# Kernel optimization log

Hardware: AMD Instinct MI355X
Metric: run time of the kernel (lower is better)

The kernel has to match this reference:

```python
import jax, jax.numpy as jnp
import numpy as np

N, E, F_IN, NCLS, H = 50000, 800000, 128, 10, 64


def setup_inputs() -> dict:
    key = jax.random.key(0)
    ks = jax.random.split(key, 24)
    p = lambda k, shp: (jax.random.normal(k, shp, dtype=jnp.float32) * 0.1)
    inp = {
        'x': jax.random.normal(ks[0], (N, F_IN), dtype=jnp.float32),
        'edge_index': jax.random.randint(ks[1], (2, E), 0, N, dtype=jnp.int64),
        'gcn1_W': p(ks[2], (F_IN, 128)), 'gcn1_b': p(ks[3], (128,)),
        'gcn2_W': p(ks[4], (128, 64)),  'gcn2_b': p(ks[5], (64,)),
        'gcn3_W': p(ks[6], (64, 32)),   'gcn3_b': p(ks[7], (32,)),
        'gat_W': p(ks[8], (32, 32)), 'gat_a_src': p(ks[9], (32,)),
        'gat_a_dst': p(ks[10], (32,)), 'gat_b': p(ks[11], (32,)),
        'lstm_Wih_f': p(ks[12], (4 * H, 32)), 'lstm_bih_f': p(ks[13], (4 * H,)), 'lstm_bhh_f': p(ks[14], (4 * H,)),
        'lstm_Wih_b': p(ks[15], (4 * H, 32)), 'lstm_bih_b': p(ks[16], (4 * H,)), 'lstm_bhh_b': p(ks[17], (4 * H,)),
        'bn_gamma': jnp.ones((2 * H,), jnp.float32), 'bn_beta': jnp.zeros((2 * H,), jnp.float32),
        'fc_W': p(ks[18], (NCLS, 2 * H)), 'fc_b': p(ks[19], (NCLS,)),
    }
    return inp


def _forward(x, edge_index, gcn1_W, gcn1_b, gcn2_W, gcn2_b, gcn3_W, gcn3_b,
             gat_W, gat_a_src, gat_a_dst, gat_b,
             lstm_Wih_f, lstm_bih_f, lstm_bhh_f, lstm_Wih_b, lstm_bih_b, lstm_bhh_b,
             bn_gamma, bn_beta, fc_W, fc_b):
    n = x.shape[0]
    loop = jnp.arange(n)
    row = jnp.concatenate([edge_index[0], loop])  # source nodes (+ self loops)
    col = jnp.concatenate([edge_index[1], loop])  # target nodes
    deg = jax.ops.segment_sum(jnp.ones_like(col, dtype=x.dtype), col, num_segments=n)
    dis = jax.lax.rsqrt(jnp.maximum(deg, 1e-12))  # deg >= 1 due to self loops
    norm = dis[row] * dis[col]

    def gcn(h, W, b):
        h = h @ W
        return jax.ops.segment_sum(h[row] * norm[:, None], col, num_segments=n) + b

    h = jax.nn.relu(gcn(x, gcn1_W, gcn1_b))
    h = jax.nn.relu(gcn(h, gcn2_W, gcn2_b))
    h = gcn(h, gcn3_W, gcn3_b)

    # GAT (1 head), self loops already in row/col, softmax over incoming edges per target
    g = h @ gat_W
    e = jax.nn.leaky_relu((g @ gat_a_src)[row] + (g @ gat_a_dst)[col], negative_slope=0.2)
    m = jax.ops.segment_max(e, col, num_segments=n)
    ee = jnp.exp(e - m[col])
    att = ee / jax.ops.segment_sum(ee, col, num_segments=n)[col]
    h = jax.ops.segment_sum(g[row] * att[:, None], col, num_segments=n) + gat_b
    h = jax.nn.relu(h)

    # bidirectional LSTM with seq_len=1, h0=c0=0 -> single cell step per direction
    def lstm_dir(xx, Wih, bih, bhh):
        gt = xx @ Wih.T + bih + bhh
        i, f, c, o = jnp.split(gt, 4, axis=-1)  # torch gate order i,f,g,o
        return jax.nn.sigmoid(o) * jnp.tanh(jax.nn.sigmoid(i) * jnp.tanh(c))

    r = jnp.concatenate([lstm_dir(h, lstm_Wih_f, lstm_bih_f, lstm_bhh_f),
                         lstm_dir(h, lstm_Wih_b, lstm_bih_b, lstm_bhh_b)], axis=-1)
    # eval mode: dropout = identity; BatchNorm1d with running_mean=0, running_var=1
    r = r * (bn_gamma / jnp.sqrt(jnp.float32(1.0 + 1e-5))) + bn_beta
    return r @ fc_W.T + fc_b


def reference(x, edge_index, gcn1_W, gcn1_b, gcn2_W, gcn2_b, gcn3_W, gcn3_b,
              gat_W, gat_a_src, gat_a_dst, gat_b,
              lstm_Wih_f, lstm_bih_f, lstm_bhh_f, lstm_Wih_b, lstm_bih_b, lstm_bhh_b,
              bn_gamma, bn_beta, fc_W, fc_b):
    return _forward(x, edge_index, gcn1_W, gcn1_b, gcn2_W, gcn2_b, gcn3_W, gcn3_b,
                    gat_W, gat_a_src, gat_a_dst, gat_b,
                    lstm_Wih_f, lstm_bih_f, lstm_bhh_f, lstm_Wih_b, lstm_bih_b, lstm_bhh_b,
                    bn_gamma, bn_beta, fc_W, fc_b)
```

## Files before the change

kernel.cpp:

```cpp
#include <hip/hip_runtime.h>
#include <hip/hip_bf16.h>
#include <math.h>

typedef __hip_bfloat16 bf16;
typedef __attribute__((ext_vector_type(8))) short short8v;
typedef __attribute__((ext_vector_type(4))) float f32x4;

#define NN 50000
#define EE 800000
#define EPB 4096
#define NBK 196
#define BCAP 6144

__device__ __forceinline__ float b2f(bf16 v) { return __bfloat162float(v); }
__device__ __forceinline__ float rcp_(float x) { return __builtin_amdgcn_rcpf(x); }
__device__ __forceinline__ float sigmoidf_(float x) { return rcp_(1.0f + __expf(-x)); }
__device__ __forceinline__ float tanhf_(float x) {
    float xx = fminf(fmaxf(x, -15.0f), 15.0f);
    float e = __expf(2.0f * xx);
    return (e - 1.0f) * rcp_(e + 1.0f);
}
__device__ __forceinline__ float leakyf_(float x) { return x > 0.0f ? x : 0.2f * x; }
__device__ __forceinline__ unsigned short f2bf(float f) {
    unsigned u = __float_as_uint(f);
    unsigned r = (u + 0x7FFFu + ((u >> 16) & 1u)) >> 16;
    return (unsigned short)r;
}
__device__ __forceinline__ unsigned pack2(float a, float b) {
    return (unsigned)f2bf(a) | ((unsigned)f2bf(b) << 16);
}
__device__ __forceinline__ float lo_(unsigned u) { return __uint_as_float(u << 16); }
__device__ __forceinline__ float hi_(unsigned u) { return __uint_as_float(u & 0xFFFF0000u); }
__device__ __forceinline__ void split4(float4 v, ushort4& hi, ushort4& lo) {
    hi.x = f2bf(v.x); lo.x = f2bf(v.x - __uint_as_float((unsigned)hi.x << 16));
    hi.y = f2bf(v.y); lo.y = f2bf(v.y - __uint_as_float((unsigned)hi.y << 16));
    hi.z = f2bf(v.z); lo.z = f2bf(v.z - __uint_as_float((unsigned)hi.z << 16));
    hi.w = f2bf(v.w); lo.w = f2bf(v.w - __uint_as_float((unsigned)hi.w << 16));
}

#define OFF_W1 0
#define OFF_B1 16384
#define OFF_W2 16512
#define OFF_B2 24704
#define OFF_W3 24768
#define OFF_B3 26816
#define OFF_GATW 26848
#define OFF_GAS 27872
#define OFF_GAD 27904
#define OFF_GAB 27936
#define OFF_WIHF 27968
#define OFF_BIHF 36160
#define OFF_BHHF 36416
#define OFF_WIHB 36672
#define OFF_BIHB 44864
#define OFF_BHHB 45120
#define OFF_GAMMA 45376
#define OFF_BETA 45504
#define OFF_FCW 45632
#define OFF_FCB 46912
#define WTOTAL 46922

struct WSrc { const void* p[20]; };

__global__ void k_detect(const unsigned short* __restrict__ xraw,
                         const unsigned int* __restrict__ eraw, int* __restrict__ flags) {
    __shared__ int f32f, i64f;
    int t = threadIdx.x;
    if (t == 0) { f32f = 0; i64f = 1; }
    __syncthreads();
    for (int i = t; i < 4096; i += 256) {
        unsigned short u = xraw[i];
        int ex = (u >> 7) & 0xFF;
        if (ex >= 0xC0) atomicOr(&f32f, 1);
        if (eraw[2 * i + 1] != 0u) atomicAnd(&i64f, 0);
    }
    __syncthreads();
    if (t == 0) { flags[0] = f32f; flags[1] = i64f; }
}

__global__ void k_cvt_w(WSrc srcs, float* __restrict__ dst, const int* __restrict__ flags,
                        int total) {
    constexpr int WOFF[21] = {OFF_W1,   OFF_B1,   OFF_W2,   OFF_B2,   OFF_W3,   OFF_B3,
                              OFF_GATW, OFF_GAS,  OFF_GAD,  OFF_GAB,  OFF_WIHF, OFF_BIHF,
                              OFF_BHHF, OFF_WIHB, OFF_BIHB, OFF_BHHB, OFF_GAMMA, OFF_BETA,
                              OFF_FCW,  OFF_FCB,  WTOTAL};
    int i = blockIdx.x * 256 + threadIdx.x;
    if (i >= total) return;
    int tn = 0;
#pragma unroll
    for (int j = 1; j < 20; ++j)
        if (i >= WOFF[j]) tn = j;
    int local = i - WOFF[tn];
    if (flags[0]) dst[i] = ((const float*)srcs.p[tn])[local];
    else dst[i] = b2f(((const bf16*)srcs.p[tn])[local]);
}

__global__ void k_prep_w1(const float* __restrict__ wp, unsigned short* __restrict__ wsplit) {
    int t = blockIdx.x * 256 + threadIdx.x;
    if (t >= 16384) return;
    int k = t >> 7, col = t & 127;
    float w = wp[OFF_W1 + k * 128 + col];
    unsigned short hi = f2bf(w);
    float hif = __uint_as_float((unsigned)hi << 16);
    unsigned short lo = f2bf(w - hif);
    int kt = k >> 5, kk = k & 31;
    wsplit[((size_t)(kt * 2 + 0) * 128 + col) * 32 + kk] = hi;
    wsplit[((size_t)(kt * 2 + 1) * 128 + col) * 32 + kk] = lo;
}

template <int KIN, int KOUT>
__global__ void k_prep_ws(const float* __restrict__ src, unsigned short* __restrict__ dst) {
    int i = blockIdx.x * 256 + threadIdx.x;
    if (i >= KIN * KOUT) return;
    int k = i / KOUT, col = i % KOUT;
    float w = src[(size_t)k * KOUT + col];
    unsigned short hi = f2bf(w);
    unsigned short lo = f2bf(w - __uint_as_float((unsigned)hi << 16));
    int kt = k >> 5, kk = k & 31;
    dst[((size_t)(kt * 2 + 0) * KOUT + col) * 32 + kk] = hi;
    dst[((size_t)(kt * 2 + 1) * KOUT + col) * 32 + kk] = lo;
}

__global__ void k_prep_wg(const float* __restrict__ wp, unsigned short* __restrict__ wsg) {
    int t = blockIdx.x * 256 + threadIdx.x;
    if (t >= 12288) return;
    int dir = t / 6144, r2 = t % 6144;
    int row = r2 >> 5, k = r2 & 31;
    int gate = row >> 6, j = row & 63;
    int srcrow = j + (gate == 1 ? 128 : (gate == 2 ? 192 : 0));
    const float* W = wp + (dir ? OFF_WIHB : OFF_WIHF);
    float w = W[(size_t)srcrow * 32 + k];
    unsigned short hi = f2bf(w);
    unsigned short lo = f2bf(w - __uint_as_float((unsigned)hi << 16));
    wsg[((size_t)(dir * 2 + 0) * 192 + row) * 32 + k] = hi;
    wsg[((size_t)(dir * 2 + 1) * 192 + row) * 32 + k] = lo;
}

__global__ __launch_bounds__(256) void k_hist(const void* __restrict__ eraw,
                                              unsigned* __restrict__ gh,
                                              const int* __restrict__ flags) {
    __shared__ int h[256];
    int t = threadIdx.x, b = blockIdx.x;
    h[t] = 0;
    __syncthreads();
    int e0 = b * EPB;
    bool i64 = flags[1] != 0;
    for (int i = t; i < EPB; i += 256) {
        int e = e0 + i;
        if (e < EE) {
            int d = i64 ? (int)((const long long*)eraw)[EE + e] : ((const int*)eraw)[EE + e];
            d = min(max(d, 0), NN - 1);
            atomicAdd(&h[d >> 8], 1);
        }
    }
    __syncthreads();
    gh[b * 256 + t] = (unsigned)h[t];
}

__global__ __launch_bounds__(256) void k_bscan(const unsigned* __restrict__ gh,
                                               unsigned* __restrict__ gh2,
                                               int* __restrict__ bb, int* __restrict__ rptr) {
    __shared__ int s[256];
    int t = threadIdx.x;
    unsigned run = 0;
    for (int blk = 0; blk < NBK; ++blk) {
        unsigned v = gh[blk * 256 + t];
        gh2[blk * 256 + t] = run;
        run += v;
    }
    s[t] = (int)run;
    __syncthreads();
    for (int o = 1; o < 256; o <<= 1) {
        int x = (t >= o) ? s[t - o] : 0;
        __syncthreads();
        s[t] += x;
        __syncthreads();
    }
    bb[t] = s[t] - (int)run;
    if (t == 0) rptr[NN] = EE;
}

__global__ __launch_bounds__(256) void k_scatter(const void* __restrict__ eraw,
                                                 const unsigned* __restrict__ gh2,
                                                 const int* __restrict__ bb,
                                                 int2* __restrict__ ebkt,
                                                 const int* __restrict__ flags) {
    __shared__ unsigned cur[256];
    int t = threadIdx.x, b = blockIdx.x;
    cur[t] = gh2[b * 256 + t] + (unsigned)bb[t];
    __syncthreads();
    int e0 = b * EPB;
    bool i64 = flags[1] != 0;
    for (int i = t; i < EPB; i += 256) {
        int e = e0 + i;
        if (e < EE) {
            int sn, d;
            if (i64) {
                sn = (int)((const long long*)eraw)[e];
                d = (int)((const long long*)eraw)[EE + e];
            } else {
                sn = ((const int*)eraw)[e];
                d = ((const int*)eraw)[EE + e];
            }
            sn = min(max(sn, 0), NN - 1);
            d = min(max(d, 0), NN - 1);
            unsigned pos = atomicAdd(&cur[d >> 8], 1u);
            if (pos < (unsigned)EE) ebkt[pos] = make_int2(sn, d);
        }
    }
}

__global__ __launch_bounds__(256) void k_bucket_csr(const int2* __restrict__ ebkt,
                                                    const int* __restrict__ bb,
                                                    int* __restrict__ rptr,
                                                    float* __restrict__ dis,
                                                    int* __restrict__ csr_src) {
    __shared__ int hist[256];
    __shared__ int excl[256];
    __shared__ int cur[256];
    __shared__ int sorted[BCAP];
    int t = threadIdx.x, b = blockIdx.x;
    int s0 = bb[b], s1 = bb[b + 1];
    int len = min(s1 - s0, BCAP);
    hist[t] = 0;
    __syncthreads();
    for (int i = t; i < len; i += 256) atomicAdd(&hist[ebkt[s0 + i].y & 255], 1);
    __syncthreads();
    int v = hist[t];
    excl[t] = v;
    __syncthreads();
    for (int o = 1; o < 256; o <<= 1) {
        int x = (t >= o) ? excl[t - o] : 0;
        __syncthreads();
        excl[t] += x;
        __syncthreads();
    }
    int loc = excl[t] - v;
    int node = b * 256 + t;
    if (node < NN) {
        rptr[node] = s0 + loc;
        dis[node] = rsqrtf((float)(v + 1));
    }
    cur[t] = loc;
    __syncthreads();
    for (int i = t; i < len; i += 256) {
        int2 p = ebkt[s0 + i];
        int pos = atomicAdd(&cur[p.y & 255], 1);
        if (pos < BCAP) sorted[pos] = p.x;
    }
    __syncthreads();
    for (int i = t; i < len; i += 256) csr_src[s0 + i] = sorted[i];
}

template <int MODE>
__global__ __launch_bounds__(256) void k_gcn1_mfma(const void* __restrict__ A,
                                                   const unsigned short* __restrict__ wsplit,
                                                   unsigned* __restrict__ C, int n,
                                                   const int* __restrict__ flags,
                                                   const float* __restrict__ dis) {
    if (flags[0] != MODE) return;
    __shared__ unsigned short Ah[64 * 136];
    __shared__ unsigned short Al[MODE ? 64 * 136 : 4];
    __shared__ unsigned short Wh[128 * 40];
    __shared__ unsigned short Wl[128 * 40];
    int t = threadIdx.x;
    int l = t & 63, w = t >> 6;
    int base = blockIdx.x * 64;
    if constexpr (MODE == 0) {
#pragma unroll
        for (int p = 0; p < 4; ++p) {
            int c = p * 256 + t;
            int nd = c >> 4, ko = (c & 15) * 8;
            int node = min(base + nd, n - 1);
            uint4 v = *(const uint4*)((const unsigned short*)A + (size_t)node * 128 + ko);
            *(uint4*)(Ah + nd * 136 + ko) = v;
        }
    } else {
#pragma unroll
        for (int p = 0; p < 8; ++p) {
            int c = p * 256 + t;
            int nd = c >> 5, ko = (c & 31) * 4;
            int node = min(base + nd, n - 1);
            float4 v = *(const float4*)((const float*)A + (size_t)node * 128 + ko);
            ushort4 hi, lo;
            split4(v, hi, lo);
            *(ushort4*)(Ah + nd * 136 + ko) = hi;
            *(ushort4*)(Al + nd * 136 + ko) = lo;
        }
    }
    int wr = (w >> 1) * 32, wc = (w & 1) * 64;
    int lrow = l & 15, lk = (l >> 4) * 8;
    f32x4 acc[2][4];
#pragma unroll
    for (int rb = 0; rb < 2; ++rb)
#pragma unroll
        for (int cb = 0; cb < 4; ++cb) acc[rb][cb] = (f32x4){0.f, 0.f, 0.f, 0.f};
    for (int kt = 0; kt < 4; ++kt) {
        __syncthreads();
#pragma unroll
        for (int p = 0; p < 2; ++p) {
            int c = p * 256 + t;
            int col = c >> 2, ko = (c & 3) * 8;
            *(uint4*)(Wh + col * 40 + ko) =
                *(const uint4*)(wsplit + ((size_t)(kt * 2 + 0) * 128 + col) * 32 + ko);
            *(uint4*)(Wl + col * 40 + ko) =
                *(const uint4*)(wsplit + ((size_t)(kt * 2 + 1) * 128 + col) * 32 + ko);
        }
        __syncthreads();
        short8v ah0 = *(const short8v*)(Ah + (wr + lrow) * 136 + kt * 32 + lk);
        short8v ah1 = *(const short8v*)(Ah + (wr + 16 + lrow) * 136 + kt * 32 + lk);
        short8v al0, al1;
        if constexpr (MODE == 1) {
            al0 = *(const short8v*)(Al + (wr + lrow) * 136 + kt * 32 + lk);
            al1 = *(const short8v*)(Al + (wr + 16 + lrow) * 136 + kt * 32 + lk);
        }
#pragma unroll
        for (int cb = 0; cb < 4; ++cb) {
            int col = wc + cb * 16 + lrow;
            short8v bh = *(const short8v*)(Wh + col * 40 + lk);
            short8v bl = *(const short8v*)(Wl + col * 40 + lk);
            acc[0][cb] = __builtin_amdgcn_mfma_f32_16x16x32_bf16(ah0, bh, acc[0][cb], 0, 0, 0);
            acc[0][cb] = __builtin_amdgcn_mfma_f32_16x16x32_bf16(ah0, bl, acc[0][cb], 0, 0, 0);
            acc[1][cb] = __builtin_amdgcn_mfma_f32_16x16x32_bf16(ah1, bh, acc[1][cb], 0, 0, 0);
            acc[1][cb] = __builtin_amdgcn_mfma_f32_16x16x32_bf16(ah1, bl, acc[1][cb], 0, 0, 0);
            if constexpr (MODE == 1) {
                acc[0][cb] = __builtin_amdgcn_mfma_f32_16x16x32_bf16(al0, bh, acc[0][cb], 0, 0, 0);
                acc[1][cb] = __builtin_amdgcn_mfma_f32_16x16x32_bf16(al1, bh, acc[1][cb], 0, 0, 0);
            }
        }
    }
#pragma unroll
    for (int rb = 0; rb < 2; ++rb) {
#pragma unroll
        for (int reg = 0; reg < 4; ++reg) {
            int row = wr + rb * 16 + (l >> 4) * 4 + reg;
            int node = base + row;
            if (node < n) {
                float sc = dis[node];
                unsigned short* cr = (unsigned short*)C + (size_t)node * 128;
#pragma unroll
                for (int cb = 0; cb < 4; ++cb) {
                    int col = wc + cb * 16 + lrow;
                    cr[col] = f2bf(acc[rb][cb][reg] * sc);
                }
            }
        }
    }
}

template <int KIN, int KOUT, bool SCALE>
__global__ __launch_bounds__(256) void k_mm_mfma(const float* __restrict__ A,
                                                 const unsigned short* __restrict__ wsplit,
                                                 unsigned short* __restrict__ C, int n,
                                                 const float* __restrict__ dis) {
    constexpr int AST = KIN + 8;
    constexpr int KT = KIN / 32;
    constexpr int CB = KOUT / 32;
    __shared__ unsigned short Ah[64 * AST];
    __shared__ unsigned short Al[64 * AST];
    __shared__ unsigned short Wh[KOUT * 40];
    __shared__ unsigned short Wl[KOUT * 40];
    int t = threadIdx.x;
    int l = t & 63, w = t >> 6;
    int base = blockIdx.x * 64;
#pragma unroll
    for (int p = 0; p < KIN / 16; ++p) {
        int c = p * 256 + t;
        int nd = c / (KIN / 4), ko = (c % (KIN / 4)) * 4;
        int node = min(base + nd, n - 1);
        float4 v = *(const float4*)(A + (size_t)node * KIN + ko);
        ushort4 hi, lo;
        split4(v, hi, lo);
        *(ushort4*)(Ah + nd * AST + ko) = hi;
        *(ushort4*)(Al + nd * AST + ko) = lo;
    }
    int wr = (w >> 1) * 32, wc = (w & 1) * (KOUT / 2);
    int lrow = l & 15, lk = (l >> 4) * 8;
    f32x4 acc[2][CB];
#pragma unroll
    for (int rb = 0; rb < 2; ++rb)
#pragma unroll
        for (int cb = 0; cb < CB; ++cb) acc[rb][cb] = (f32x4){0.f, 0.f, 0.f, 0.f};
    for (int kt = 0; kt < KT; ++kt) {
        __syncthreads();
        for (int c = t; c < KOUT * 4; c += 256) {
            int col = c >> 2, ko = (c & 3) * 8;
            *(uint4*)(Wh + col * 40 + ko) =
                *(const uint4*)(wsplit + ((size_t)(kt * 2 + 0) * KOUT + col) * 32 + ko);
            *(uint4*)(Wl + col * 40 + ko) =
                *(const uint4*)(wsplit + ((size_t)(kt * 2 + 1) * KOUT + col) * 32 + ko);
        }
        __syncthreads();
        short8v ah0 = *(const short8v*)(Ah + (wr + lrow) * AST + kt * 32 + lk);
        short8v ah1 = *(const short8v*)(Ah + (wr + 16 + lrow) * AST + kt * 32 + lk);
        short8v al0 = *(const short8v*)(Al + (wr + lrow) * AST + kt * 32 + lk);
        short8v al1 = *(const short8v*)(Al + (wr + 16 + lrow) * AST + kt * 32 + lk);
#pragma unroll
        for (int cb = 0; cb < CB; ++cb) {
            int col = wc + cb * 16 + lrow;
            short8v bh = *(const short8v*)(Wh + col * 40 + lk);
            short8v bl = *(const short8v*)(Wl + col * 40 + lk);
            acc[0][cb] = __builtin_amdgcn_mfma_f32_16x16x32_bf16(ah0, bh, acc[0][cb], 0, 0, 0);
            acc[0][cb] = __builtin_amdgcn_mfma_f32_16x16x32_bf16(ah0, bl, acc[0][cb], 0, 0, 0);
            acc[0][cb] = __builtin_amdgcn_mfma_f32_16x16x32_bf16(al0, bh, acc[0][cb], 0, 0, 0);
            acc[1][cb] = __builtin_amdgcn_mfma_f32_16x16x32_bf16(ah1, bh, acc[1][cb], 0, 0, 0);
            acc[1][cb] = __builtin_amdgcn_mfma_f32_16x16x32_bf16(ah1, bl, acc[1][cb], 0, 0, 0);
            acc[1][cb] = __builtin_amdgcn_mfma_f32_16x16x32_bf16(al1, bh, acc[1][cb], 0, 0, 0);
        }
    }
#pragma unroll
    for (int rb = 0; rb < 2; ++rb) {
#pragma unroll
        for (int reg = 0; reg < 4; ++reg) {
            int row = wr + rb * 16 + (l >> 4) * 4 + reg;
            int node = base + row;
            if (node < n) {
                float sc = SCALE ? dis[node] : 1.0f;
                unsigned short* cr = C + (size_t)node * KOUT;
#pragma unroll
                for (int cb = 0; cb < CB; ++cb) {
                    int col = wc + cb * 16 + lrow;
                    cr[col] = f2bf(acc[rb][cb][reg] * sc);
                }
            }
        }
    }
}

template <bool RELU>
__global__ void k_agg128(const unsigned* __restrict__ t, const int* __restrict__ rptr,
                         const int* __restrict__ csr_src, const float* __restrict__ dis,
                         const float* __restrict__ bias, float* __restrict__ out, int n) {
    int wave = (blockIdx.x * blockDim.x + threadIdx.x) >> 6;
    int lane = threadIdx.x & 63;
    if (wave >= n) return;
    int dst = wave;
    float dd = dis[dst];
    float ax, ay;
    {
        unsigned u = t[(size_t)dst * 64 + lane];
        ax = lo_(u);
        ay = hi_(u);
    }
    int s = __builtin_amdgcn_readfirstlane(max(0, min(rptr[dst], EE)));
    int e = __builtin_amdgcn_readfirstlane(max(s, min(rptr[dst + 1], EE)));
    int j = s;
    for (; j + 8 <= e; j += 8) {
        int i0 = csr_src[j], i1 = csr_src[j + 1], i2 = csr_src[j + 2], i3 = csr_src[j + 3];
        int i4 = csr_src[j + 4], i5 = csr_src[j + 5], i6 = csr_src[j + 6], i7 = csr_src[j + 7];
        unsigned u0 = t[(size_t)i0 * 64 + lane], u1 = t[(size_t)i1 * 64 + lane];
        unsigned u2 = t[(size_t)i2 * 64 + lane], u3 = t[(size_t)i3 * 64 + lane];
        unsigned u4 = t[(size_t)i4 * 64 + lane], u5 = t[(size_t)i5 * 64 + lane];
        unsigned u6 = t[(size_t)i6 * 64 + lane], u7 = t[(size_t)i7 * 64 + lane];
        ax += (lo_(u0) + lo_(u1)) + (lo_(u2) + lo_(u3)) + (lo_(u4) + lo_(u5)) + (lo_(u6) + lo_(u7));
        ay += (hi_(u0) + hi_(u1)) + (hi_(u2) + hi_(u3)) + (hi_(u4) + hi_(u5)) + (hi_(u6) + hi_(u7));
    }
    for (; j + 4 <= e; j += 4) {
        int i0 = csr_src[j], i1 = csr_src[j + 1], i2 = csr_src[j + 2], i3 = csr_src[j + 3];
        unsigned u0 = t[(size_t)i0 * 64 + lane], u1 = t[(size_t)i1 * 64 + lane];
        unsigned u2 = t[(size_t)i2 * 64 + lane], u3 = t[(size_t)i3 * 64 + lane];
        ax += (lo_(u0) + lo_(u1)) + (lo_(u2) + lo_(u3));
        ay += (hi_(u0) + hi_(u1)) + (hi_(u2) + hi_(u3));
    }
    for (; j < e; ++j) {
        unsigned u0 = t[(size_t)csr_src[j] * 64 + lane];
        ax += lo_(u0);
        ay += hi_(u0);
    }
    float2 bv = *(const float2*)(bias + 2 * lane);
    float vx = ax * dd + bv.x;
    float vy = ay * dd + bv.y;
    if (RELU) { vx = fmaxf(vx, 0.f); vy = fmaxf(vy, 0.f); }
    *(float2*)(out + (size_t)dst * 128 + 2 * lane) = make_float2(vx, vy);
}

template <bool RELU>
__global__ void k_agg64(const unsigned* __restrict__ t, const int* __restrict__ rptr,
                        const int* __restrict__ csr_src, const float* __restrict__ dis,
                        const float* __restrict__ bias, float* __restrict__ out, int n) {
    int wave = (blockIdx.x * blockDim.x + threadIdx.x) >> 6;
    int lane = threadIdx.x & 63;
    if (wave >= n) return;
    int dst = wave;
    int half = lane >> 5, l32 = lane & 31;
    float dd = dis[dst];
    float ax = 0.f, ay = 0.f;
    if (!half) {
        unsigned u = t[(size_t)dst * 32 + l32];
        ax = lo_(u);
        ay = hi_(u);
    }
    int s = max(0, min(rptr[dst], EE));
    int e = max(s, min(rptr[dst + 1], EE));
    int cnt = e - s;
    int pairs = cnt >> 1;
    int p = 0;
    for (; p + 4 <= pairs; p += 4) {
        int jb = s + 2 * p + half;
        int i0 = csr_src[jb], i1 = csr_src[jb + 2], i2 = csr_src[jb + 4], i3 = csr_src[jb + 6];
        unsigned u0 = t[(size_t)i0 * 32 + l32], u1 = t[(size_t)i1 * 32 + l32];
        unsigned u2 = t[(size_t)i2 * 32 + l32], u3 = t[(size_t)i3 * 32 + l32];
        ax += (lo_(u0) + lo_(u1)) + (lo_(u2) + lo_(u3));
        ay += (hi_(u0) + hi_(u1)) + (hi_(u2) + hi_(u3));
    }
    for (; p < pairs; ++p) {
        int i0 = csr_src[s + 2 * p + half];
        unsigned u0 = t[(size_t)i0 * 32 + l32];
        ax += lo_(u0);
        ay += hi_(u0);
    }
    if ((cnt & 1) && !half) {
        unsigned u0 = t[(size_t)csr_src[e - 1] * 32 + l32];
        ax += lo_(u0);
        ay += hi_(u0);
    }
    ax += __shfl_down(ax, 32);
    ay += __shfl_down(ay, 32);
    if (!half) {
        float2 bv = *(const float2*)(bias + 2 * l32);
        float vx = ax * dd + bv.x;
        float vy = ay * dd + bv.y;
        if (RELU) { vx = fmaxf(vx, 0.f); vy = fmaxf(vy, 0.f); }
        *(float2*)(out + (size_t)dst * 64 + 2 * l32) = make_float2(vx, vy);
    }
}

template <bool RELU>
__global__ void k_agg32(const unsigned* __restrict__ t, const int* __restrict__ rptr,
                        const int* __restrict__ csr_src, const float* __restrict__ dis,
                        const float* __restrict__ bias, float* __restrict__ out, int n) {
    int wave = (blockIdx.x * blockDim.x + threadIdx.x) >> 6;
    int lane = threadIdx.x & 63;
    if (wave >= n) return;
    int dst = wave;
    int q = lane >> 4, l16 = lane & 15;
    float dd = dis[dst];
    float ax = 0.f, ay = 0.f;
    if (q == 0) {
        unsigned u = t[(size_t)dst * 16 + l16];
        ax = lo_(u);
        ay = hi_(u);
    }
    int s = max(0, min(rptr[dst], EE));
    int e = max(s, min(rptr[dst + 1], EE));
    int cnt = e - s;
    int quads = cnt >> 2;
    int p = 0;
    for (; p + 4 <= quads; p += 4) {
        int jb = s + 4 * p + q;
        int i0 = csr_src[jb], i1 = csr_src[jb + 4], i2 = csr_src[jb + 8], i3 = csr_src[jb + 12];
        unsigned u0 = t[(size_t)i0 * 16 + l16], u1 = t[(size_t)i1 * 16 + l16];
        unsigned u2 = t[(size_t)i2 * 16 + l16], u3 = t[(size_t)i3 * 16 + l16];
        ax += (lo_(u0) + lo_(u1)) + (lo_(u2) + lo_(u3));
        ay += (hi_(u0) + hi_(u1)) + (hi_(u2) + hi_(u3));
    }
    for (; p < quads; ++p) {
        int i0 = csr_src[s + 4 * p + q];
        unsigned u0 = t[(size_t)i0 * 16 + l16];
        ax += lo_(u0);
        ay += hi_(u0);
    }
    int rem = cnt - 4 * quads;
    if (q < rem) {
        unsigned u0 = t[(size_t)csr_src[s + 4 * quads + q] * 16 + l16];
        ax += lo_(u0);
        ay += hi_(u0);
    }
    ax += __shfl_down(ax, 32);
    ay += __shfl_down(ay, 32);
    ax += __shfl_down(ax, 16);
    ay += __shfl_down(ay, 16);
    if (q == 0) {
        float2 bv = *(const float2*)(bias + 2 * l16);
        float vx = ax * dd + bv.x;
        float vy = ay * dd + bv.y;
        if (RELU) { vx = fmaxf(vx, 0.f); vy = fmaxf(vy, 0.f); }
        *(float2*)(out + (size_t)dst * 32 + 2 * l16) = make_float2(vx, vy);
    }
}

__global__ void k_gat_vec(const unsigned* __restrict__ g, const float* __restrict__ a_src,
                          const float* __restrict__ a_dst, float* __restrict__ asrc,
                          float* __restrict__ adst, int n) {
    int i = blockIdx.x * 256 + threadIdx.x;
    if (i >= n) return;
    float s = 0.0f, d = 0.0f;
    const unsigned* gr = g + (size_t)i * 16;
#pragma unroll
    for (int k = 0; k < 16; ++k) {
        unsigned u = gr[k];
        float v0 = lo_(u), v1 = hi_(u);
        s += v0 * a_src[2 * k] + v1 * a_src[2 * k + 1];
        d += v0 * a_dst[2 * k] + v1 * a_dst[2 * k + 1];
    }
    asrc[i] = s;
    adst[i] = d;
}

__global__ void k_gat_agg(const unsigned* __restrict__ g, const int* __restrict__ rptr,
                          const int* __restrict__ csr_src, const float* __restrict__ asrc,
                          const float* __restrict__ adst, const float* __restrict__ gat_b,
                          float* __restrict__ out, int n) {
    int wave = (blockIdx.x * blockDim.x + threadIdx.x) >> 6;
    int lane = threadIdx.x & 63;
    if (wave >= n) return;
    int dst = wave;
    int q = lane >> 4, l16 = lane & 15;
    float ad = adst[dst];
    int s = max(0, min(rptr[dst], EE));
    int e = max(s, min(rptr[dst + 1], EE));
    float ax = 0.f, ay = 0.f, denom = 0.f;
    if (q == 0) {
        float w0 = __expf(fminf(leakyf_(asrc[dst] + ad), 80.f));
        unsigned u = g[(size_t)dst * 16 + l16];
        ax = lo_(u) * w0;
        ay = hi_(u) * w0;
        denom = w0;
    }
    int cnt = e - s;
    int quads = cnt >> 2;
    int p = 0;
    for (; p + 4 <= quads; p += 4) {
        int jb = s + 4 * p + q;
        int i0 = csr_src[jb], i1 = csr_src[jb + 4], i2 = csr_src[jb + 8], i3 = csr_src[jb + 12];
        float a0 = asrc[i0], a1 = asrc[i1], a2 = asrc[i2], a3 = asrc[i3];
        unsigned u0 = g[(size_t)i0 * 16 + l16], u1 = g[(size_t)i1 * 16 + l16];
        unsigned u2 = g[(size_t)i2 * 16 + l16], u3 = g[(size_t)i3 * 16 + l16];
        float w0 = __expf(fminf(leakyf_(a0 + ad), 80.f));
        float w1 = __expf(fminf(leakyf_(a1 + ad), 80.f));
        float w2 = __expf(fminf(leakyf_(a2 + ad), 80.f));
        float w3 = __expf(fminf(leakyf_(a3 + ad), 80.f));
        denom += (w0 + w1) + (w2 + w3);
        ax += lo_(u0) * w0 + lo_(u1) * w1 + lo_(u2) * w2 + lo_(u3) * w3;
        ay += hi_(u0) * w0 + hi_(u1) * w1 + hi_(u2) * w2 + hi_(u3) * w3;
    }
    for (; p < quads; ++p) {
        int i0 = csr_src[s + 4 * p + q];
        float wgt = __expf(fminf(leakyf_(asrc[i0] + ad), 80.f));
        unsigned u0 = g[(size_t)i0 * 16 + l16];
        denom += wgt;
        ax += lo_(u0) * wgt;
        ay += hi_(u0) * wgt;
    }
    int rem = cnt - 4 * quads;
    if (q < rem) {
        int i0 = csr_src[s + 4 * quads + q];
        float wgt = __expf(fminf(leakyf_(asrc[i0] + ad), 80.f));
        unsigned u0 = g[(size_t)i0 * 16 + l16];
        denom += wgt;
        ax += lo_(u0) * wgt;
        ay += hi_(u0) * wgt;
    }
    ax += __shfl_down(ax, 32);
    ay += __shfl_down(ay, 32);
    denom += __shfl_down(denom, 32);
    ax += __shfl_down(ax, 16);
    ay += __shfl_down(ay, 16);
    denom += __shfl_down(denom, 16);
    if (q == 0) {
        float r = rcp_(denom);
        float vx = fmaxf(ax * r + gat_b[2 * l16], 0.f);
        float vy = fmaxf(ay * r + gat_b[2 * l16 + 1], 0.f);
        *(float2*)(out + (size_t)dst * 32 + 2 * l16) = make_float2(vx, vy);
    }
}

__global__ __launch_bounds__(256) void k_gates_mfma(const float* __restrict__ h,
                                                    const unsigned short* __restrict__ wsg,
                                                    const float* __restrict__ wp,
                                                    float* __restrict__ rbufT, int n) {
    __shared__ unsigned short Ah[64 * 40];
    __shared__ unsigned short Al[64 * 40];
    __shared__ unsigned short Wh[192 * 40];
    __shared__ unsigned short Wl[192 * 40];
    __shared__ float bI[64], bG[64], bO[64], gs[64], gb[64];
    int t = threadIdx.x;
    int dir = blockIdx.y;
    int l = t & 63, w = t >> 6;
    int base = blockIdx.x * 64;
#pragma unroll
    for (int p = 0; p < 2; ++p) {
        int c = p * 256 + t;
        int nd = c >> 3, ko = (c & 7) * 4;
        int node = min(base + nd, n - 1);
        float4 v = *(const float4*)(h + (size_t)node * 32 + ko);
        ushort4 hi, lo;
        split4(v, hi, lo);
        *(ushort4*)(Ah + nd * 40 + ko) = hi;
        *(ushort4*)(Al + nd * 40 + ko) = lo;
    }
    {
        const unsigned short* sh = wsg + (size_t)(dir * 2 + 0) * 192 * 32;
        const unsigned short* sl = wsg + (size_t)(dir * 2 + 1) * 192 * 32;
#pragma unroll
        for (int p = 0; p < 3; ++p) {
            int c = p * 256 + t;
            int row = c >> 2, ko = (c & 3) * 8;
            *(uint4*)(Wh + row * 40 + ko) = *(const uint4*)(sh + (size_t)row * 32 + ko);
            *(uint4*)(Wl + row * 40 + ko) = *(const uint4*)(sl + (size_t)row * 32 + ko);
        }
    }
    if (t < 64) {
        const float* bi_ = wp + (dir ? OFF_BIHB : OFF_BIHF);
        const float* bh_ = wp + (dir ? OFF_BHHB : OFF_BHHF);
        bI[t] = bi_[t] + bh_[t];
        bG[t] = bi_[128 + t] + bh_[128 + t];
        bO[t] = bi_[192 + t] + bh_[192 + t];
        gs[t] = wp[OFF_GAMMA + dir * 64 + t] * rsqrtf(1.0f + 1e-5f);
        gb[t] = wp[OFF_BETA + dir * 64 + t];
    }
    __syncthreads();
    int lrow = l & 15, lk = (l >> 4) * 8;
    short8v hh = *(const short8v*)(Ah + (w * 16 + lrow) * 40 + lk);
    short8v hl = *(const short8v*)(Al + (w * 16 + lrow) * 40 + lk);
    f32x4 acc[12];
#pragma unroll
    for (int m = 0; m < 12; ++m) acc[m] = (f32x4){0.f, 0.f, 0.f, 0.f};
#pragma unroll
    for (int m = 0; m < 12; ++m) {
        short8v wh = *(const short8v*)(Wh + (m * 16 + lrow) * 40 + lk);
        short8v wl = *(const short8v*)(Wl + (m * 16 + lrow) * 40 + lk);
        acc[m] = __builtin_amdgcn_mfma_f32_16x16x32_bf16(wh, hh, acc[m], 0, 0, 0);
        acc[m] = __builtin_amdgcn_mfma_f32_16x16x32_bf16(wl, hh, acc[m], 0, 0, 0);
        acc[m] = __builtin_amdgcn_mfma_f32_16x16x32_bf16(wh, hl, acc[m], 0, 0, 0);
    }
    int node = base + w * 16 + lrow;
    if (node < n) {
#pragma unroll
        for (int m = 0; m < 4; ++m) {
#pragma unroll
            for (int reg = 0; reg < 4; ++reg) {
                int j = 16 * m + (l >> 4) * 4 + reg;
                float iv = acc[m][reg] + bI[j];
                float gv = acc[m + 4][reg] + bG[j];
                float ov = acc[m + 8][reg] + bO[j];
                float v = sigmoidf_(ov) * tanhf_(sigmoidf_(iv) * tanhf_(gv));
                rbufT[(size_t)(dir * 64 + j) * NN + node] = v * gs[j] + gb[j];
            }
        }
    }
}

__global__ __launch_bounds__(256) void k_fc(const float* __restrict__ rbufT,
                                            const float* __restrict__ wp,
                                            void* __restrict__ out,
                                            const int* __restrict__ flags, int n) {
    __shared__ float rs[64 * 129];
    __shared__ float ps[4 * 640];
    int t = threadIdx.x;
    int base = blockIdx.x * 64;
    for (int i = t; i < 8192; i += 256) {
        int jj = i >> 6, nd = i & 63;
        int node = min(base + nd, n - 1);
        rs[nd * 129 + jj] = rbufT[(size_t)jj * NN + node];
    }
    __syncthreads();
    {
        int nd = t & 63, quarter = t >> 6;
        const float* fcw = wp + OFF_FCW;
        int jbase = quarter * 32;
        float p10[10];
#pragma unroll
        for (int c = 0; c < 10; ++c) p10[c] = 0.f;
#pragma unroll 4
        for (int k = 0; k < 32; ++k) {
            float r = rs[nd * 129 + jbase + k];
#pragma unroll
            for (int c = 0; c < 10; ++c) p10[c] += r * fcw[c * 128 + jbase + k];
        }
#pragma unroll
        for (int c = 0; c < 10; ++c) ps[quarter * 640 + nd * 10 + c] = p10[c];
    }
    __syncthreads();
    bool f32o = flags[0] != 0;
    for (int idx = t; idx < 640; idx += 256) {
        int gnode = base + idx / 10;
        if (gnode < n) {
            int c = idx % 10;
            float v = wp[OFF_FCB + c] + ps[idx] + ps[640 + idx] + ps[1280 + idx] + ps[1920 + idx];
            if (f32o) ((float*)out)[(size_t)base * 10 + idx] = v;
            else ((unsigned short*)out)[(size_t)base * 10 + idx] = f2bf(v);
        }
    }
}

extern "C" void kernel_launch(void* const* d_in, const int* in_sizes, int n_in,
                              void* d_out, int out_size, void* d_ws, size_t ws_size,
                              hipStream_t stream) {
    const int N = NN;

    char* w = (char*)d_ws;
    auto alloc = [&](size_t bytes) {
        void* p = (void*)w;
        w += (bytes + 255) & ~(size_t)255;
        return p;
    };
    int* flags = (int*)alloc(256);
    float* wpool = (float*)alloc((size_t)WTOTAL * 4);
    unsigned short* wsplit = (unsigned short*)alloc(65536);
    unsigned short* ws2 = (unsigned short*)alloc(32768);
    unsigned short* ws3 = (unsigned short*)alloc(8192);
    unsigned short* wsgat = (unsigned short*)alloc(4096);
    unsigned short* wsg = (unsigned short*)alloc(49152);
    float* dis = (float*)alloc((size_t)N * 4);
    int* rptr = (int*)alloc((size_t)(N + 1) * 4);
    int* csr_src = (int*)alloc((size_t)EE * 4);
    unsigned* gh = (unsigned*)alloc((size_t)NBK * 256 * 4);
    unsigned* gh2 = (unsigned*)alloc((size_t)NBK * 256 * 4);
    int* bb = (int*)alloc(1024);
    int2* ebkt = (int2*)alloc((size_t)EE * 8);
    float* asrc = (float*)alloc((size_t)N * 4);
    float* adst = (float*)alloc((size_t)N * 4);
    unsigned* bufT = (unsigned*)alloc((size_t)N * 64 * 4);
    float* bufH = (float*)alloc((size_t)N * 128 * 4);
    float* rbufT = (float*)alloc((size_t)N * 128 * 4);

    WSrc ws_srcs;
    for (int i = 0; i < 20; ++i) ws_srcs.p[i] = d_in[2 + i];

    const int NB = (N + 255) / 256;
    const int AGG = (N + 3) / 4;
    const int TMB = (N + 63) / 64;
    const int WB = (WTOTAL + 255) / 256;

    k_detect<<<1, 256, 0, stream>>>((const unsigned short*)d_in[0],
                                    (const unsigned int*)d_in[1], flags);
    k_cvt_w<<<WB, 256, 0, stream>>>(ws_srcs, wpool, flags, WTOTAL);
    k_prep_w1<<<64, 256, 0, stream>>>(wpool, wsplit);
    k_prep_ws<128, 64><<<32, 256, 0, stream>>>(wpool + OFF_W2, ws2);
    k_prep_ws<64, 32><<<8, 256, 0, stream>>>(wpool + OFF_W3, ws3);
    k_prep_ws<32, 32><<<4, 256, 0, stream>>>(wpool + OFF_GATW, wsgat);
    k_prep_wg<<<48, 256, 0, stream>>>(wpool, wsg);
    k_hist<<<NBK, 256, 0, stream>>>(d_in[1], gh, flags);
    k_bscan<<<1, 256, 0, stream>>>(gh, gh2, bb, rptr);
    k_scatter<<<NBK, 256, 0, stream>>>(d_in[1], gh2, bb, ebkt, flags);
    k_bucket_csr<<<NBK, 256, 0, stream>>>(ebkt, bb, rptr, dis, csr_src);

    k_gcn1_mfma<0><<<TMB, 256, 0, stream>>>(d_in[0], wsplit, bufT, N, flags, dis);
    k_gcn1_mfma<1><<<TMB, 256, 0, stream>>>(d_in[0], wsplit, bufT, N, flags, dis);
    k_agg128<true><<<AGG, 256, 0, stream>>>(bufT, rptr, csr_src, dis, wpool + OFF_B1, bufH, N);
    k_mm_mfma<128, 64, true><<<TMB, 256, 0, stream>>>(bufH, ws2, (unsigned short*)bufT, N, dis);
    k_agg64<true><<<AGG, 256, 0, stream>>>(bufT, rptr, csr_src, dis, wpool + OFF_B2, bufH, N);
    k_mm_mfma<64, 32, true><<<TMB, 256, 0, stream>>>(bufH, ws3, (unsigned short*)bufT, N, dis);
    k_agg32<false><<<AGG, 256, 0, stream>>>(bufT, rptr, csr_src, dis, wpool + OFF_B3, bufH, N);
    k_mm_mfma<32, 32, false><<<TMB, 256, 0, stream>>>(bufH, wsgat, (unsigned short*)bufT, N, dis);
    k_gat_vec<<<NB, 256, 0, stream>>>(bufT, wpool + OFF_GAS, wpool + OFF_GAD, asrc, adst, N);
    k_gat_agg<<<AGG, 256, 0, stream>>>(bufT, rptr, csr_src, asrc, adst, wpool + OFF_GAB, bufH, N);
    k_gates_mfma<<<dim3(TMB, 2), 256, 0, stream>>>(bufH, wsg, wpool, rbufT, N);
    k_fc<<<TMB, 256, 0, stream>>>(rbufT, wpool, d_out, flags, N);
}
```

Baseline: 353.6 us.

## Fuse weight prep kernels, GAT matmul with attention vectors, and LSTM with FC

Merges the five weight-split prep kernels into one launch. Fuses the GAT projection matmul with the per-node attention dot products, so g is not re-read from global memory. Fuses both LSTM directions with batchnorm and the final FC in one block, keeping the 128-wide LSTM output in shared memory instead of a transposed global buffer. This removes several launches and roughly 50 MB of intermediate traffic, at the cost of larger shared memory use per block, lower occupancy, and serialised per-direction weight loads.

```diff
diff --git a/kernel.cpp b/kernel.cpp
--- a/kernel.cpp
+++ b/kernel.cpp
@@ -95,45 +95,58 @@
     else dst[i] = b2f(((const bf16*)srcs.p[tn])[local]);
 }
 
-__global__ void k_prep_w1(const float* __restrict__ wp, unsigned short* __restrict__ wsplit) {
-    int t = blockIdx.x * 256 + threadIdx.x;
-    if (t >= 16384) return;
-    int k = t >> 7, col = t & 127;
-    float w = wp[OFF_W1 + k * 128 + col];
-    unsigned short hi = f2bf(w);
-    float hif = __uint_as_float((unsigned)hi << 16);
-    unsigned short lo = f2bf(w - hif);
-    int kt = k >> 5, kk = k & 31;
-    wsplit[((size_t)(kt * 2 + 0) * 128 + col) * 32 + kk] = hi;
-    wsplit[((size_t)(kt * 2 + 1) * 128 + col) * 32 + kk] = lo;
-}
-
-template <int KIN, int KOUT>
-__global__ void k_prep_ws(const float* __restrict__ src, unsigned short* __restrict__ dst) {
+__global__ void k_prep_all(const float* __restrict__ wp, unsigned short* __restrict__ w1,
+                           unsigned short* __restrict__ w2, unsigned short* __restrict__ w3,
+                           unsigned short* __restrict__ wgat, unsigned short* __restrict__ wg) {
     int i = blockIdx.x * 256 + threadIdx.x;
-    if (i >= KIN * KOUT) return;
-    int k = i / KOUT, col = i % KOUT;
-    float w = src[(size_t)k * KOUT + col];
-    unsigned short hi = f2bf(w);
-    unsigned short lo = f2bf(w - __uint_as_float((unsigned)hi << 16));
-    int kt = k >> 5, kk = k & 31;
-    dst[((size_t)(kt * 2 + 0) * KOUT + col) * 32 + kk] = hi;
-    dst[((size_t)(kt * 2 + 1) * KOUT + col) * 32 + kk] = lo;
-}
-
-__global__ void k_prep_wg(const float* __restrict__ wp, unsigned short* __restrict__ wsg) {
-    int t = blockIdx.x * 256 + threadIdx.x;
-    if (t >= 12288) return;
-    int dir = t / 6144, r2 = t % 6144;
-    int row = r2 >> 5, k = r2 & 31;
-    int gate = row >> 6, j = row & 63;
-    int srcrow = j + (gate == 1 ? 128 : (gate == 2 ? 192 : 0));
-    const float* W = wp + (dir ? OFF_WIHB : OFF_WIHF);
-    float w = W[(size_t)srcrow * 32 + k];
-    unsigned short hi = f2bf(w);
-    unsigned short lo = f2bf(w - __uint_as_float((unsigned)hi << 16));
-    wsg[((size_t)(dir * 2 + 0) * 192 + row) * 32 + k] = hi;
-    wsg[((size_t)(dir * 2 + 1) * 192 + row) * 32 + k] = lo;
+    if (i < 16384) {
+        int k = i >> 7, col = i & 127;
+        float v = wp[OFF_W1 + k * 128 + col];
+        unsigned short hi = f2bf(v);
+        unsigned short lo = f2bf(v - __uint_as_float((unsigned)hi << 16));
+        int kt = k >> 5, kk = k & 31;
+        w1[((size_t)(kt * 2 + 0) * 128 + col) * 32 + kk] = hi;
+        w1[((size_t)(kt * 2 + 1) * 128 + col) * 32 + kk] = lo;
+    } else if (i < 24576) {
+        int j = i - 16384;
+        int k = j >> 6, col = j & 63;
+        float v = wp[OFF_W2 + k * 64 + col];
+        unsigned short hi = f2bf(v);
+        unsigned short lo = f2bf(v - __uint_as_float((unsigned)hi << 16));
+        int kt = k >> 5, kk = k & 31;
+        w2[((size_t)(kt * 2 + 0) * 64 + col) * 32 + kk] = hi;
+        w2[((size_t)(kt * 2 + 1) * 64 + col) * 32 + kk] = lo;
+    } else if (i < 26624) {
+        int j = i - 24576;
+        int k = j >> 5, col = j & 31;
+        float v = wp[OFF_W3 + k * 32 + col];
+        unsigned short hi = f2bf(v);
+        unsigned short lo = f2bf(v - __uint_as_float((unsigned)hi << 16));
+        int kt = k >> 5, kk = k & 31;
+        w3[((size_t)(kt * 2 + 0) * 32 + col) * 32 + kk] = hi;
+        w3[((size_t)(kt * 2 + 1) * 32 + col) * 32 + kk] = lo;
+    } else if (i < 27648) {
+        int j = i - 26624;
+        int k = j >> 5, col = j & 31;
+        float v = wp[OFF_GATW + k * 32 + col];
+        unsigned short hi = f2bf(v);
+        unsigned short lo = f2bf(v - __uint_as_float((unsigned)hi << 16));
+        int kk = k & 31;
+        wgat[((size_t)col) * 32 + kk] = hi;
+        wgat[((size_t)(32 + col)) * 32 + kk] = lo;
+    } else if (i < 39936) {
+        int j = i - 27648;
+        int dir = j / 6144, r2 = j % 6144;
+        int row = r2 >> 5, k = r2 & 31;
+        int gate = row >> 6, jj = row & 63;
+        int srcrow = jj + (gate == 1 ? 128 : (gate == 2 ? 192 : 0));
+        const float* W = wp + (dir ? OFF_WIHB : OFF_WIHF);
+        float v = W[(size_t)srcrow * 32 + k];
+        unsigned short hi = f2bf(v);
+        unsigned short lo = f2bf(v - __uint_as_float((unsigned)hi << 16));
+        wg[((size_t)(dir * 2 + 0) * 192 + row) * 32 + k] = hi;
+        wg[((size_t)(dir * 2 + 1) * 192 + row) * 32 + k] = lo;
+    }
 }
 
 __global__ __launch_bounds__(256) void k_hist(const void* __restrict__ eraw,
@@ -427,6 +440,78 @@
     }
 }
 
+__global__ __launch_bounds__(256) void k_mm_gat(const float* __restrict__ A,
+                                                const unsigned short* __restrict__ wsplit,
+                                                unsigned short* __restrict__ C, int n,
+                                                const float* __restrict__ wp,
+                                                float* __restrict__ asrc,
+                                                float* __restrict__ adst) {
+    __shared__ unsigned short Ah[64 * 40];
+    __shared__ unsigned short Al[64 * 40];
+    __shared__ unsigned short Wh[32 * 40];
+    __shared__ unsigned short Wl[32 * 40];
+    __shared__ float gsh[64 * 33];
+    int t = threadIdx.x;
+    int l = t & 63, w = t >> 6;
+    int base = blockIdx.x * 64;
+#pragma unroll
+    for (int p = 0; p < 2; ++p) {
+        int c = p * 256 + t;
+        int nd = c >> 3, ko = (c & 7) * 4;
+        int node = min(base + nd, n - 1);
+        float4 v = *(const float4*)(A + (size_t)node * 32 + ko);
+        ushort4 hi, lo;
+        split4(v, hi, lo);
+        *(ushort4*)(Ah + nd * 40 + ko) = hi;
+        *(ushort4*)(Al + nd * 40 + ko) = lo;
+    }
+    if (t < 128) {
+        int col = t >> 2, ko = (t & 3) * 8;
+        *(uint4*)(Wh + col * 40 + ko) = *(const uint4*)(wsplit + ((size_t)col) * 32 + ko);
+        *(uint4*)(Wl + col * 40 + ko) = *(const uint4*)(wsplit + ((size_t)(32 + col)) * 32 + ko);
+    }
+    __syncthreads();
+    int wr = (w >> 1) * 32, wc = (w & 1) * 16;
+    int lrow = l & 15, lk = (l >> 4) * 8;
+    short8v ah0 = *(const short8v*)(Ah + (wr + lrow) * 40 + lk);
+    short8v ah1 = *(const short8v*)(Ah + (wr + 16 + lrow) * 40 + lk);
+    short8v al0 = *(const short8v*)(Al + (wr + lrow) * 40 + lk);
+    short8v al1 = *(const short8v*)(Al + (wr + 16 + lrow) * 40 + lk);
+    short8v bh = *(const short8v*)(Wh + (wc + lrow) * 40 + lk);
+    short8v bl = *(const short8v*)(Wl + (wc + lrow) * 40 + lk);
+    f32x4 acc0 = (f32x4){0.f, 0.f, 0.f, 0.f}, acc1 = (f32x4){0.f, 0.f, 0.f, 0.f};
+    acc0 = __builtin_amdgcn_mfma_f32_16x16x32_bf16(ah0, bh, acc0, 0, 0, 0);
+    acc0 = __builtin_amdgcn_mfma_f32_16x16x32_bf16(ah0, bl, acc0, 0, 0, 0);
+    acc0 = __builtin_amdgcn_mfma_f32_16x16x32_bf16(al0, bh, acc0, 0, 0, 0);
+    acc1 = __builtin_amdgcn_mfma_f32_16x16x32_bf16(ah1, bh, acc1, 0, 0, 0);
+    acc1 = __builtin_amdgcn_mfma_f32_16x16x32_bf16(ah1, bl, acc1, 0, 0, 0);
+    acc1 = __builtin_amdgcn_mfma_f32_16x16x32_bf16(al1, bh, acc1, 0, 0, 0);
+#pragma unroll
+    for (int rb = 0; rb < 2; ++rb) {
+#pragma unroll
+        for (int reg = 0; reg < 4; ++reg) {
+            int row = wr + rb * 16 + (l >> 4) * 4 + reg;
+            int node = base + row;
+            float v = rb ? acc1[reg] : acc0[reg];
+            unsigned short b16 = f2bf(v);
+            gsh[row * 33 + wc + lrow] = __uint_as_float((unsigned)b16 << 16);
+            if (node < n) C[(size_t)node * 32 + wc + lrow] = b16;
+        }
+    }
+    __syncthreads();
+    if (t < 64) {
+        int node = base + t;
+        float s = 0.f, d = 0.f;
+#pragma unroll
+        for (int c = 0; c < 32; ++c) {
+            float gv = gsh[t * 33 + c];
+            s += gv * wp[OFF_GAS + c];
+            d += gv * wp[OFF_GAD + c];
+        }
+        if (node < n) { asrc[node] = s; adst[node] = d; }
+    }
+}
+
 template <bool RELU>
 __global__ void k_agg128(const unsigned* __restrict__ t, const int* __restrict__ rptr,
                          const int* __restrict__ csr_src, const float* __restrict__ dis,
@@ -577,24 +662,6 @@
         if (RELU) { vx = fmaxf(vx, 0.f); vy = fmaxf(vy, 0.f); }
         *(float2*)(out + (size_t)dst * 32 + 2 * l16) = make_float2(vx, vy);
     }
-}
-
-__global__ void k_gat_vec(const unsigned* __restrict__ g, const float* __restrict__ a_src,
-                          const float* __restrict__ a_dst, float* __restrict__ asrc,
-                          float* __restrict__ adst, int n) {
-    int i = blockIdx.x * 256 + threadIdx.x;
-    if (i >= n) return;
-    float s = 0.0f, d = 0.0f;
-    const unsigned* gr = g + (size_t)i * 16;
-#pragma unroll
-    for (int k = 0; k < 16; ++k) {
-        unsigned u = gr[k];
-        float v0 = lo_(u), v1 = hi_(u);
-        s += v0 * a_src[2 * k] + v1 * a_src[2 * k + 1];
-        d += v0 * a_dst[2 * k] + v1 * a_dst[2 * k + 1];
-    }
-    asrc[i] = s;
-    adst[i] = d;
 }
 
 __global__ void k_gat_agg(const unsigned* __restrict__ g, const int* __restrict__ rptr,
@@ -665,23 +732,23 @@
     }
 }
 
-__global__ __launch_bounds__(256) void k_gates_mfma(const float* __restrict__ h,
-                                                    const unsigned short* __restrict__ wsg,
-                                                    const float* __restrict__ wp,
-                                                    float* __restrict__ rbufT, int n) {
+__global__ __launch_bounds__(256) void k_lstm_full(const float* __restrict__ h,
+                                                   const unsigned short* __restrict__ wsg,
+                                                   const float* __restrict__ wp,
+                                                   void* __restrict__ out,
+                                                   const int* __restrict__ flags, int n) {
     __shared__ unsigned short Ah[64 * 40];
     __shared__ unsigned short Al[64 * 40];
     __shared__ unsigned short Wh[192 * 40];
     __shared__ unsigned short Wl[192 * 40];
-    __shared__ float bI[64], bG[64], bO[64], gs[64], gb[64];
-    int t = threadIdx.x;
-    int dir = blockIdx.y;
-    int l = t & 63, w = t >> 6;
+    __shared__ float rs[64 * 129];
+    __shared__ float bI[2][64], bG[2][64], bO[2][64], gsc[2][64], gbe[2][64];
+    float* ps = (float*)Wh;
+    int t = threadIdx.x, l = t & 63, w = t >> 6;
     int base = blockIdx.x * 64;
 #pragma unroll
     for (int p = 0; p < 2; ++p) {
-        int c = p * 256 + t;
-        int nd = c >> 3, ko = (c & 7) * 4;
+        int c = p * 256 + t, nd = c >> 3, ko = (c & 7) * 4;
         int node = min(base + nd, n - 1);
         float4 v = *(const float4*)(h + (size_t)node * 32 + ko);
         ushort4 hi, lo;
@@ -689,70 +756,66 @@
         *(ushort4*)(Ah + nd * 40 + ko) = hi;
         *(ushort4*)(Al + nd * 40 + ko) = lo;
     }
+    if (t < 128) {
+        int dir = t >> 6, j = t & 63;
+        const float* bi_ = wp + (dir ? OFF_BIHB : OFF_BIHF);
+        const float* bh_ = wp + (dir ? OFF_BHHB : OFF_BHHF);
+        bI[dir][j] = bi_[j] + bh_[j];
+        bG[dir][j] = bi_[128 + j] + bh_[128 + j];
+        bO[dir][j] = bi_[192 + j] + bh_[192 + j];
+        gsc[dir][j] = wp[OFF_GAMMA + dir * 64 + j] * rsqrtf(1.0f + 1e-5f);
+        gbe[dir][j] = wp[OFF_BETA + dir * 64 + j];
+    }
     {
-        const unsigned short* sh = wsg + (size_t)(dir * 2 + 0) * 192 * 32;
-        const unsigned short* sl = wsg + (size_t)(dir * 2 + 1) * 192 * 32;
+        const unsigned short* sh = wsg;
+        const unsigned short* sl = wsg + (size_t)192 * 32;
 #pragma unroll
         for (int p = 0; p < 3; ++p) {
-            int c = p * 256 + t;
-            int row = c >> 2, ko = (c & 3) * 8;
+            int c = p * 256 + t, row = c >> 2, ko = (c & 3) * 8;
             *(uint4*)(Wh + row * 40 + ko) = *(const uint4*)(sh + (size_t)row * 32 + ko);
             *(uint4*)(Wl + row * 40 + ko) = *(const uint4*)(sl + (size_t)row * 32 + ko);
         }
-    }
-    if (t < 64) {
-        const float* bi_ = wp + (dir ? OFF_BIHB : OFF_BIHF);
-        const float* bh_ = wp + (dir ? OFF_BHHB : OFF_BHHF);
-        bI[t] = bi_[t] + bh_[t];
-        bG[t] = bi_[128 + t] + bh_[128 + t];
-        bO[t] = bi_[192 + t] + bh_[192 + t];
-        gs[t] = wp[OFF_GAMMA + dir * 64 + t] * rsqrtf(1.0f + 1e-5f);
-        gb[t] = wp[OFF_BETA + dir * 64 + t];
     }
     __syncthreads();
     int lrow = l & 15, lk = (l >> 4) * 8;
     short8v hh = *(const short8v*)(Ah + (w * 16 + lrow) * 40 + lk);
     short8v hl = *(const short8v*)(Al + (w * 16 + lrow) * 40 + lk);
-    f32x4 acc[12];
-#pragma unroll
-    for (int m = 0; m < 12; ++m) acc[m] = (f32x4){0.f, 0.f, 0.f, 0.f};
-#pragma unroll
-    for (int m = 0; m < 12; ++m) {
-        short8v wh = *(const short8v*)(Wh + (m * 16 + lrow) * 40 + lk);
-        short8v wl = *(const short8v*)(Wl + (m * 16 + lrow) * 40 + lk);
-        acc[m] = __builtin_amdgcn_mfma_f32_16x16x32_bf16(wh, hh, acc[m], 0, 0, 0);
-        acc[m] = __builtin_amdgcn_mfma_f32_16x16x32_bf16(wl, hh, acc[m], 0, 0, 0);
-        acc[m] = __builtin_amdgcn_mfma_f32_16x16x32_bf16(wh, hl, acc[m], 0, 0, 0);
-    }
-    int node = base + w * 16 + lrow;
-    if (node < n) {
+    for (int dir = 0; dir < 2; ++dir) {
+        if (dir == 1) {
+            __syncthreads();
+            const unsigned short* sh = wsg + (size_t)2 * 192 * 32;
+            const unsigned short* sl = wsg + (size_t)3 * 192 * 32;
+#pragma unroll
+            for (int p = 0; p < 3; ++p) {
+                int c = p * 256 + t, row = c >> 2, ko = (c & 3) * 8;
+                *(uint4*)(Wh + row * 40 + ko) = *(const uint4*)(sh + (size_t)row * 32 + ko);
+                *(uint4*)(Wl + row * 40 + ko) = *(const uint4*)(sl + (size_t)row * 32 + ko);
+            }
+            __syncthreads();
+        }
+        f32x4 acc[12];
+#pragma unroll
+        for (int m = 0; m < 12; ++m) acc[m] = (f32x4){0.f, 0.f, 0.f, 0.f};
+#pragma unroll
+        for (int m = 0; m < 12; ++m) {
+            short8v wh_ = *(const short8v*)(Wh + (m * 16 + lrow) * 40 + lk);
+            short8v wl_ = *(const short8v*)(Wl + (m * 16 + lrow) * 40 + lk);
+            acc[m] = __builtin_amdgcn_mfma_f32_16x16x32_bf16(wh_, hh, acc[m], 0, 0, 0);
+            acc[m] = __builtin_amdgcn_mfma_f32_16x16x32_bf16(wl_, hh, acc[m], 0, 0, 0);
+            acc[m] = __builtin_amdgcn_mfma_f32_16x16x32_bf16(wh_, hl, acc[m], 0, 0, 0);
+        }
 #pragma unroll
         for (int m = 0; m < 4; ++m) {
 #pragma unroll
             for (int reg = 0; reg < 4; ++reg) {
                 int j = 16 * m + (l >> 4) * 4 + reg;
-                float iv = acc[m][reg] + bI[j];
-                float gv = acc[m + 4][reg] + bG[j];
-                float ov = acc[m + 8][reg] + bO[j];
+                float iv = acc[m][reg] + bI[dir][j];
+                float gv = acc[m + 4][reg] + bG[dir][j];
+                float ov = acc[m + 8][reg] + bO[dir][j];
                 float v = sigmoidf_(ov) * tanhf_(sigmoidf_(iv) * tanhf_(gv));
-                rbufT[(size_t)(dir * 64 + j) * NN + node] = v * gs[j] + gb[j];
+                rs[(w * 16 + lrow) * 129 + dir * 64 + j] = v * gsc[dir][j] + gbe[dir][j];
             }
         }
-    }
-}
-
-__global__ __launch_bounds__(256) void k_fc(const float* __restrict__ rbufT,
-                                            const float* __restrict__ wp,
-                                            void* __restrict__ out,
-                                            const int* __restrict__ flags, int n) {
-    __shared__ float rs[64 * 129];
-    __shared__ float ps[4 * 640];
-    int t = threadIdx.x;
-    int base = blockIdx.x * 64;
-    for (int i = t; i < 8192; i += 256) {
-        int jj = i >> 6, nd = i & 63;
-        int node = min(base + nd, n - 1);
-        rs[nd * 129 + jj] = rbufT[(size_t)jj * NN + node];
     }
     __syncthreads();
     {
@@ -813,12 +876,10 @@
     float* adst = (float*)alloc((size_t)N * 4);
     unsigned* bufT = (unsigned*)alloc((size_t)N * 64 * 4);
     float* bufH = (float*)alloc((size_t)N * 128 * 4);
-    float* rbufT = (float*)alloc((size_t)N * 128 * 4);
 
     WSrc ws_srcs;
     for (int i = 0; i < 20; ++i) ws_srcs.p[i] = d_in[2 + i];
 
-    const int NB = (N + 255) / 256;
     const int AGG = (N + 3) / 4;
     const int TMB = (N + 63) / 64;
     const int WB = (WTOTAL + 255) / 256;
@@ -826,11 +887,7 @@
     k_detect<<<1, 256, 0, stream>>>((const unsigned short*)d_in[0],
                                     (const unsigned int*)d_in[1], flags);
     k_cvt_w<<<WB, 256, 0, stream>>>(ws_srcs, wpool, flags, WTOTAL);
-    k_prep_w1<<<64, 256, 0, stream>>>(wpool, wsplit);
-    k_prep_ws<128, 64><<<32, 256, 0, stream>>>(wpool + OFF_W2, ws2);
-    k_prep_ws<64, 32><<<8, 256, 0, stream>>>(wpool + OFF_W3, ws3);
-    k_prep_ws<32, 32><<<4, 256, 0, stream>>>(wpool + OFF_GATW, wsgat);
-    k_prep_wg<<<48, 256, 0, stream>>>(wpool, wsg);
+    k_prep_all<<<156, 256, 0, stream>>>(wpool, wsplit, ws2, ws3, wsgat, wsg);
     k_hist<<<NBK, 256, 0, stream>>>(d_in[1], gh, flags);
     k_bscan<<<1, 256, 0, stream>>>(gh, gh2, bb, rptr);
     k_scatter<<<NBK, 256, 0, stream>>>(d_in[1], gh2, bb, ebkt, flags);
@@ -843,9 +900,7 @@
     k_agg64<true><<<AGG, 256, 0, stream>>>(bufT, rptr, csr_src, dis, wpool + OFF_B2, bufH, N);
     k_mm_mfma<64, 32, true><<<TMB, 256, 0, stream>>>(bufH, ws3, (unsigned short*)bufT, N, dis);
     k_agg32<false><<<AGG, 256, 0, stream>>>(bufT, rptr, csr_src, dis, wpool + OFF_B3, bufH, N);
-    k_mm_mfma<32, 32, false><<<TMB, 256, 0, stream>>>(bufH, wsgat, (unsigned short*)bufT, N, dis);
-    k_gat_vec<<<NB, 256, 0, stream>>>(bufT, wpool + OFF_GAS, wpool + OFF_GAD, asrc, adst, N);
+    k_mm_gat<<<TMB, 256, 0, stream>>>(bufH, wsgat, (unsigned short*)bufT, N, wpool, asrc, adst);
     k_gat_agg<<<AGG, 256, 0, stream>>>(bufT, rptr, csr_src, asrc, adst, wpool + OFF_GAB, bufH, N);
-    k_gates_mfma<<<dim3(TMB, 2), 256, 0, stream>>>(bufH, wsg, wpool, rbufT, N);
-    k_fc<<<TMB, 256, 0, stream>>>(rbufT, wpool, d_out, flags, N);
-}
+    k_lstm_full<<<TMB, 256, 0, stream>>>(bufH, wsg, wpool, d_out, flags, N);
+}
```

Result: faster. 333.3 us (-5.7%).
